# Kernel optimization log

Hardware: AMD Instinct MI355X
Metric: run time of the kernel (lower is better)

## Reference

```python
import jax, jax.numpy as jnp
import numpy as np

# Module constants (from init_kwargs / derived)
KH, KW = 3, 3
STRIDE = (1, 1)
PAD = (1, 1)
DIL = (1, 1)
N_OFFSET_GRPS = 8  # offset.shape[1] // (2*KH*KW) = 144 // 18
N_WEIGHT_GRPS = 1


def setup_inputs() -> dict:
    key = jax.random.key(0)
    k1, k2, k3, k4, k5 = jax.random.split(key, 5)
    B, C, H, W = 4, 64, 128, 128
    inp = {
        "input": jax.random.normal(k1, (B, C, H, W), dtype=jnp.float32),
        "offset": jax.random.normal(k2, (B, 2 * N_OFFSET_GRPS * KH * KW, H, W), dtype=jnp.float32),
        "mask": jax.random.uniform(k3, (B, N_OFFSET_GRPS * KH * KW, H, W), dtype=jnp.float32),
        "weight": jax.random.normal(k4, (64, C, KH, KW), dtype=jnp.float32) * 0.05,
        "bias": jax.random.normal(k5, (64,), dtype=jnp.float32) * 0.05,
    }
    return inp


def _deform_conv2d(x, offset, mask, weight, bias):
    B, C, H, W = x.shape
    Ho, Wo = offset.shape[2], offset.shape[3]
    G = N_OFFSET_GRPS
    K = KH * KW
    Cg = C // G

    # base (un-deformed) sampling positions per kernel tap and output pixel
    ky, kx = jnp.meshgrid(jnp.arange(KH), jnp.arange(KW), indexing="ij")
    ky = ky.reshape(K)
    kx = kx.reshape(K)
    oy = jnp.arange(Ho) * STRIDE[0] - PAD[0]
    ox = jnp.arange(Wo) * STRIDE[1] - PAD[1]
    base_y = (oy[None, :, None] + (ky * DIL[0])[:, None, None]).astype(x.dtype)  # [K,Ho,1]
    base_x = (ox[None, None, :] + (kx * DIL[1])[:, None, None]).astype(x.dtype)  # [K,1,Wo]

    off = offset.reshape(B, G, K, 2, Ho, Wo)  # [...,0]=dy, [...,1]=dx
    py = base_y[None, None] + off[:, :, :, 0]  # [B,G,K,Ho,Wo]
    px = base_x[None, None] + off[:, :, :, 1]

    y0 = jnp.floor(py)
    x0 = jnp.floor(px)
    ly = py - y0  # fractional parts
    lx = px - x0
    y0i = y0.astype(jnp.int32)
    x0i = x0.astype(jnp.int32)

    xg = x.reshape(B, G, Cg, H * W)  # per-offset-group channel slices

    def corner(yi, xi):
        valid = ((yi >= 0) & (yi < H) & (xi >= 0) & (xi < W)).astype(x.dtype)
        idx = jnp.clip(yi, 0, H - 1) * W + jnp.clip(xi, 0, W - 1)  # [B,G,K,Ho,Wo]
        gather = lambda xbg, ibg: xbg[:, ibg]  # [Cg,H*W],[K,Ho,Wo] -> [Cg,K,Ho,Wo]
        v = jax.vmap(jax.vmap(gather))(xg, idx)  # [B,G,Cg,K,Ho,Wo]
        return v * valid[:, :, None]

    w00 = (1 - ly) * (1 - lx)
    w01 = (1 - ly) * lx
    w10 = ly * (1 - lx)
    w11 = ly * lx
    samp = (corner(y0i, x0i) * w00[:, :, None]
            + corner(y0i, x0i + 1) * w01[:, :, None]
            + corner(y0i + 1, x0i) * w10[:, :, None]
            + corner(y0i + 1, x0i + 1) * w11[:, :, None])  # [B,G,Cg,K,Ho,Wo]

    samp = samp * mask.reshape(B, G, 1, K, Ho, Wo)  # DCNv2 modulation
    col = samp.reshape(B, C, K, Ho, Wo)
    wr = weight.reshape(weight.shape[0], C, K)  # groups == 1
    out = jnp.einsum("ock,bckhw->bohw", wr, col) + bias[None, :, None, None]
    return out


def reference(input, offset, mask, weight, bias):
    return _deform_conv2d(input, offset, mask, weight, bias)
```

## Files before the change

### kernel.cpp

```cpp
#include <hip/hip_runtime.h>

#define HH 128
#define WW 128
#define CC 64
#define CO 64
#define BB 4
#define GG 8
#define CG 8
#define KK 9
#define HW (HH*WW)
#define PXT 32
#define NC 3
#define FRAG 512

typedef __attribute__((ext_vector_type(8))) short short8;
typedef __attribute__((ext_vector_type(4))) float floatx4;

union S8I { short8 s; int i[4]; };

__device__ inline short f2bf(float f) {
    union { float f; unsigned u; } v; v.f = f;
    return (short)((v.u + 0x7FFF + ((v.u >> 16) & 1)) >> 16);
}
__device__ inline unsigned rnd_bf(float f) {
    union { float f; unsigned u; } v; v.f = f;
    return v.u + 0x7FFF + ((v.u >> 16) & 1);
}
__device__ inline float bflo(int e) { union { int i; float f; } u; u.i = e << 16; return u.f; }
__device__ inline float bfhi(int e) { union { int i; float f; } u; u.i = e & 0xffff0000; return u.f; }

__global__ __launch_bounds__(256)
void wt_prepack(const float* __restrict__ wt, short* __restrict__ wf) {
    const int tid = blockIdx.x * 256 + threadIdx.x;
    if (tid >= GG * NC * 4 * FRAG) return;
    const int j  = tid & 7;
    const int L  = (tid >> 3) & 63;
    const int fid = tid >> 9;
    const int ot = fid & 3;
    const int gc = fid >> 2;
    const int c  = gc % 3;
    const int g  = gc / 3;
    const int kp = c * 32 + (L >> 4) * 8 + j;
    const int o  = ot * 16 + (L & 15);
    float val = 0.f;
    if (kp < 72) {
        const int kk = kp >> 3;
        const int cg = kp & 7;
        val = wt[o * 576 + (g * 8 + cg) * 9 + kk];
    }
    wf[tid] = f2bf(val);
}

__global__ __launch_bounds__(256)
void in_transpose(const float* __restrict__ in, short* __restrict__ in_t) {
    const int p = blockIdx.x * 256 + threadIdx.x;
    const int g = blockIdx.y, b = blockIdx.z;
    const float* src = in + (b * CC + g * CG) * HW + p;
    short8 v;
    #pragma unroll
    for (int cg = 0; cg < CG; ++cg) v[cg] = f2bf(src[cg * HW]);
    *(short8*)(in_t + ((b * GG + g) * HW + p) * 8) = v;
}

__global__ __launch_bounds__(256, 6)
void dcn_fused(const short* __restrict__ in_t, const float* __restrict__ off,
               const float* __restrict__ msk, const short* __restrict__ wf,
               const float* __restrict__ bias, float* __restrict__ out)
{
    __shared__ short s_w[NC * 4 * FRAG];
    __shared__ short s_col[NC * 2 * FRAG];
    __shared__ float s_bias[64];

    const int pxbase = blockIdx.x * PXT;
    const int ho = blockIdx.y;
    const int b  = blockIdx.z;
    const int t  = threadIdx.x;
    const int w = t >> 6, lane = t & 63;
    const int s  = w & 1;
    const int oh = w >> 1;

    if (t < 64) s_bias[t] = bias[t];
    for (int idx = t; idx < 384; idx += 256) {
        const int pt = idx / 192, r = idx - pt * 192;
        ((int*)s_col)[(4 + pt) * 256 + 64 + r] = 0;
    }
    __syncthreads();

    floatx4 acc[2];
    #pragma unroll
    for (int i = 0; i < 2; ++i)
        #pragma unroll
        for (int r = 0; r < 4; ++r)
            acc[i][r] = s_bias[(oh * 2 + i) * 16 + (lane >> 4) * 4 + r];

    const short* inb = in_t + (long)b * GG * HW * 8;

    for (int g = 0; g < GG; ++g) {
        __syncthreads();

        {
            const short8* wsrc = (const short8*)(wf + g * (NC * 4 * FRAG));
            short8* wdst = (short8*)s_w;
            #pragma unroll
            for (int i = t; i < NC * 4 * 64; i += 256) wdst[i] = wsrc[i];
        }

        const short* ing = inb + g * HW * 8;
        for (int pidx = t; pidx < KK * PXT; pidx += 256) {
            const int kk = pidx >> 5;
            const int pl = pidx & 31;
            const int px = pxbase + pl;
            const int ky = kk / 3, kx = kk - ky * 3;

            const int offc = (b * 144 + g * 18 + kk * 2) * HW + ho * WW + px;
            const float dy = off[offc];
            const float dx = off[offc + HW];
            const float m  = msk[(b * 72 + g * 9 + kk) * HW + ho * WW + px];

            const float py  = (float)(ho - 1 + ky) + dy;
            const float pxf = (float)(px - 1 + kx) + dx;
            const float y0f = floorf(py), x0f = floorf(pxf);
            const float ly = py - y0f, lx = pxf - x0f;
            const int y0 = (int)y0f, x0 = (int)x0f;
            const int y1 = y0 + 1,  x1 = x0 + 1;

            const float vy0 = (y0 >= 0 && y0 < HH) ? 1.f : 0.f;
            const float vy1 = (y1 >= 0 && y1 < HH) ? 1.f : 0.f;
            const float vx0 = (x0 >= 0 && x0 < WW) ? 1.f : 0.f;
            const float vx1 = (x1 >= 0 && x1 < WW) ? 1.f : 0.f;
            const int y0c = min(max(y0, 0), HH - 1), y1c = min(max(y1, 0), HH - 1);
            const int x0c = min(max(x0, 0), WW - 1), x1c = min(max(x1, 0), WW - 1);

            const float w00 = (1.f - ly) * (1.f - lx) * vy0 * vx0 * m;
            const float w01 = (1.f - ly) * lx         * vy0 * vx1 * m;
            const float w10 = ly         * (1.f - lx) * vy1 * vx0 * m;
            const float w11 = ly         * lx         * vy1 * vx1 * m;

            S8I u00, u01, u10, u11;
            u00.s = *(const short8*)(ing + (y0c * WW + x0c) * 8);
            u01.s = *(const short8*)(ing + (y0c * WW + x1c) * 8);
            u10.s = *(const short8*)(ing + (y1c * WW + x0c) * 8);
            u11.s = *(const short8*)(ing + (y1c * WW + x1c) * 8);

            S8I res;
            #pragma unroll
            for (int pc = 0; pc < 4; ++pc) {
                const int e00 = u00.i[pc], e01 = u01.i[pc];
                const int e10 = u10.i[pc], e11 = u11.i[pc];
                const float vx_ = w00 * bflo(e00) + w01 * bflo(e01)
                                + w10 * bflo(e10) + w11 * bflo(e11);
                const float vy_ = w00 * bfhi(e00) + w01 * bfhi(e01)
                                + w10 * bfhi(e10) + w11 * bfhi(e11);
                res.i[pc] = (int)__builtin_amdgcn_perm(rnd_bf(vy_), rnd_bf(vx_), 0x07060302u);
            }

            const int c = kk >> 2, q = kk & 3;
            const int pt = pl >> 4, n = pl & 15;
            *(short8*)(s_col + ((c * 2 + pt) * 64 + q * 16 + n) * 8) = res.s;
        }

        __syncthreads();

        #pragma unroll
        for (int c = 0; c < NC; ++c) {
            const short8 bfr = *(const short8*)&s_col[((c * 2 + s) * 64 + lane) * 8];
            #pragma unroll
            for (int i = 0; i < 2; ++i) {
                const short8 afr = *(const short8*)&s_w[((c * 4 + oh * 2 + i) * 64 + lane) * 8];
                acc[i] = __builtin_amdgcn_mfma_f32_16x16x32_bf16(afr, bfr, acc[i], 0, 0, 0);
            }
        }
    }

    const int q4 = lane >> 4, n = lane & 15;
    const int px = pxbase + s * 16 + n;
    #pragma unroll
    for (int i = 0; i < 2; ++i)
        #pragma unroll
        for (int r = 0; r < 4; ++r) {
            const int o = (oh * 2 + i) * 16 + q4 * 4 + r;
            out[((b * CO + o) * HH + ho) * WW + px] = acc[i][r];
        }
}

extern "C" void kernel_launch(void* const* d_in, const int* in_sizes, int n_in,
                              void* d_out, int out_size, void* d_ws, size_t ws_size,
                              hipStream_t stream) {
    const float* in   = (const float*)d_in[0];
    const float* off  = (const float*)d_in[1];
    const float* msk  = (const float*)d_in[2];
    const float* wt   = (const float*)d_in[3];
    const float* bias = (const float*)d_in[4];
    float* out = (float*)d_out;
    short* wf   = (short*)d_ws;
    short* in_t = (short*)d_ws + 49152;

    wt_prepack<<<192, 256, 0, stream>>>(wt, wf);
    in_transpose<<<dim3(HW / 256, GG, BB), 256, 0, stream>>>(in, in_t);

    dim3 grid(WW / PXT, HH, BB);
    dcn_fused<<<grid, 256, 0, stream>>>(in_t, off, msk, wf, bias, out);
}
```

Measured before the change: 155.8 us.

## Restructure DCN kernel: prefetch offsets, sample all groups once, single-sync MFMA pass

Halves the pixel tile to 16 and drops the per-group loop with its two barriers. All offset and mask values are prefetched into registers up front, the whole im2col tile for every group is built in one pass, and a single barrier precedes the MFMA loop. Weight fragments are read straight from global memory instead of being staged in LDS, and two accumulators alternate to break the MFMA dependency chain. The costs are more registers (launch bounds lowered to 4), twice the blocks, and global weight loads repeated per block.

```diff
diff --git a/kernel.cpp b/kernel.cpp
--- a/kernel.cpp
+++ b/kernel.cpp
@@ -9,9 +9,10 @@
 #define CG 8
 #define KK 9
 #define HW (HH*WW)
-#define PXT 32
+#define PXT 16
 #define NC 3
 #define FRAG 512
+#define NPOS (GG*KK*PXT)
 
 typedef __attribute__((ext_vector_type(8))) short short8;
 typedef __attribute__((ext_vector_type(4))) float floatx4;
@@ -62,63 +63,58 @@
     *(short8*)(in_t + ((b * GG + g) * HW + p) * 8) = v;
 }
 
-__global__ __launch_bounds__(256, 6)
+__global__ __launch_bounds__(256, 4)
 void dcn_fused(const short* __restrict__ in_t, const float* __restrict__ off,
                const float* __restrict__ msk, const short* __restrict__ wf,
                const float* __restrict__ bias, float* __restrict__ out)
 {
-    __shared__ short s_w[NC * 4 * FRAG];
-    __shared__ short s_col[NC * 2 * FRAG];
-    __shared__ float s_bias[64];
+    __shared__ short s_col[GG * NC * FRAG];
 
     const int pxbase = blockIdx.x * PXT;
     const int ho = blockIdx.y;
     const int b  = blockIdx.z;
     const int t  = threadIdx.x;
     const int w = t >> 6, lane = t & 63;
-    const int s  = w & 1;
-    const int oh = w >> 1;
 
-    if (t < 64) s_bias[t] = bias[t];
+    float pdy[5], pdx[5], pm[5];
+    #pragma unroll
+    for (int i = 0; i < 5; ++i) {
+        const int pidx = t + i * 256;
+        if (pidx < NPOS) {
+            const int tc = pidx >> 4;
+            const int g  = tc / 9, kk = tc - g * 9;
+            const int px = pxbase + (pidx & 15);
+            const int base = ho * WW + px;
+            const int offc = (b * 144 + g * 18 + kk * 2) * HW + base;
+            pdy[i] = off[offc];
+            pdx[i] = off[offc + HW];
+            pm[i]  = msk[(b * 72 + g * 9 + kk) * HW + base];
+        }
+    }
+
     for (int idx = t; idx < 384; idx += 256) {
-        const int pt = idx / 192, r = idx - pt * 192;
-        ((int*)s_col)[(4 + pt) * 256 + 64 + r] = 0;
+        const int g = idx / 48, l = (idx - g * 48) + 16;
+        ((int4*)s_col)[(g * 3 + 2) * 64 + l] = make_int4(0, 0, 0, 0);
     }
-    __syncthreads();
 
-    floatx4 acc[2];
+    const int q4 = lane >> 4, n16 = lane & 15;
+    floatx4 acc0, acc1;
     #pragma unroll
-    for (int i = 0; i < 2; ++i)
-        #pragma unroll
-        for (int r = 0; r < 4; ++r)
-            acc[i][r] = s_bias[(oh * 2 + i) * 16 + (lane >> 4) * 4 + r];
+    for (int r = 0; r < 4; ++r) { acc0[r] = bias[w * 16 + q4 * 4 + r]; acc1[r] = 0.f; }
 
     const short* inb = in_t + (long)b * GG * HW * 8;
-
-    for (int g = 0; g < GG; ++g) {
-        __syncthreads();
-
-        {
-            const short8* wsrc = (const short8*)(wf + g * (NC * 4 * FRAG));
-            short8* wdst = (short8*)s_w;
-            #pragma unroll
-            for (int i = t; i < NC * 4 * 64; i += 256) wdst[i] = wsrc[i];
-        }
-
-        const short* ing = inb + g * HW * 8;
-        for (int pidx = t; pidx < KK * PXT; pidx += 256) {
-            const int kk = pidx >> 5;
-            const int pl = pidx & 31;
+    #pragma unroll
+    for (int i = 0; i < 5; ++i) {
+        const int pidx = t + i * 256;
+        if (pidx < NPOS) {
+            const int tc = pidx >> 4;
+            const int g  = tc / 9, kk = tc - g * 9;
+            const int pl = pidx & 15;
             const int px = pxbase + pl;
             const int ky = kk / 3, kx = kk - ky * 3;
 
-            const int offc = (b * 144 + g * 18 + kk * 2) * HW + ho * WW + px;
-            const float dy = off[offc];
-            const float dx = off[offc + HW];
-            const float m  = msk[(b * 72 + g * 9 + kk) * HW + ho * WW + px];
-
-            const float py  = (float)(ho - 1 + ky) + dy;
-            const float pxf = (float)(px - 1 + kx) + dx;
+            const float py  = (float)(ho - 1 + ky) + pdy[i];
+            const float pxf = (float)(px - 1 + kx) + pdx[i];
             const float y0f = floorf(py), x0f = floorf(pxf);
             const float ly = py - y0f, lx = pxf - x0f;
             const int y0 = (int)y0f, x0 = (int)x0f;
@@ -131,11 +127,13 @@
             const int y0c = min(max(y0, 0), HH - 1), y1c = min(max(y1, 0), HH - 1);
             const int x0c = min(max(x0, 0), WW - 1), x1c = min(max(x1, 0), WW - 1);
 
+            const float m = pm[i];
             const float w00 = (1.f - ly) * (1.f - lx) * vy0 * vx0 * m;
             const float w01 = (1.f - ly) * lx         * vy0 * vx1 * m;
             const float w10 = ly         * (1.f - lx) * vy1 * vx0 * m;
             const float w11 = ly         * lx         * vy1 * vx1 * m;
 
+            const short* ing = inb + g * (HW * 8);
             S8I u00, u01, u10, u11;
             u00.s = *(const short8*)(ing + (y0c * WW + x0c) * 8);
             u01.s = *(const short8*)(ing + (y0c * WW + x1c) * 8);
@@ -155,32 +153,26 @@
             }
 
             const int c = kk >> 2, q = kk & 3;
-            const int pt = pl >> 4, n = pl & 15;
-            *(short8*)(s_col + ((c * 2 + pt) * 64 + q * 16 + n) * 8) = res.s;
-        }
-
-        __syncthreads();
-
-        #pragma unroll
-        for (int c = 0; c < NC; ++c) {
-            const short8 bfr = *(const short8*)&s_col[((c * 2 + s) * 64 + lane) * 8];
-            #pragma unroll
-            for (int i = 0; i < 2; ++i) {
-                const short8 afr = *(const short8*)&s_w[((c * 4 + oh * 2 + i) * 64 + lane) * 8];
-                acc[i] = __builtin_amdgcn_mfma_f32_16x16x32_bf16(afr, bfr, acc[i], 0, 0, 0);
-            }
+            *(short8*)(s_col + ((g * 3 + c) * 64 + q * 16 + pl) * 8) = res.s;
         }
     }
 
-    const int q4 = lane >> 4, n = lane & 15;
-    const int px = pxbase + s * 16 + n;
+    __syncthreads();
+
     #pragma unroll
-    for (int i = 0; i < 2; ++i)
-        #pragma unroll
-        for (int r = 0; r < 4; ++r) {
-            const int o = (oh * 2 + i) * 16 + q4 * 4 + r;
-            out[((b * CO + o) * HH + ho) * WW + px] = acc[i][r];
-        }
+    for (int gc = 0; gc < GG * NC; ++gc) {
+        const short8 bfr = *(const short8*)&s_col[(gc * 64 + lane) * 8];
+        const short8 afr = *(const short8*)&wf[((gc * 4 + w) * 64 + lane) * 8];
+        if (gc & 1) acc1 = __builtin_amdgcn_mfma_f32_16x16x32_bf16(afr, bfr, acc1, 0, 0, 0);
+        else        acc0 = __builtin_amdgcn_mfma_f32_16x16x32_bf16(afr, bfr, acc0, 0, 0, 0);
+    }
+
+    const int px = pxbase + n16;
+    #pragma unroll
+    for (int r = 0; r < 4; ++r) {
+        const int o = w * 16 + q4 * 4 + r;
+        out[((b * CO + o) * HH + ho) * WW + px] = acc0[r] + acc1[r];
+    }
 }
 
 extern "C" void kernel_launch(void* const* d_in, const int* in_sizes, int n_in,
```

After: 146.4 us. 1.06x faster.
